# Kernel optimization log

Hardware: AMD Instinct MI355X
Metric: run time of the kernel (lower is better)

Reference implementation:

```python
import jax, jax.numpy as jnp
import numpy as np

N, E, FN, FE, L, G = 4096, 16384, 16, 8, 128, 64
EPS = 1e-5


def setup_inputs() -> dict:
    key = jax.random.key(0)
    ks = iter(jax.random.split(key, 40))

    def lin_w(shape):
        return jax.random.normal(next(ks), shape, jnp.float32) * (1.0 / np.sqrt(shape[0]))

    d = {}
    d["x"] = jax.random.normal(next(ks), (N, FN), jnp.float32)
    d["edge_attr"] = jax.random.normal(next(ks), (E, FE), jnp.float32)
    d["edge_index"] = jax.random.randint(next(ks), (2, E), 0, N)
    d["batch"] = jnp.sort(jax.random.randint(next(ks), (N,), 0, G))
    for i, (cin, cout) in enumerate([(FN, 32), (32, 64), (64, 128)], 1):
        d[f"We{i}"] = lin_w((FE, cin * cout))          # edge_fc weight
        d[f"be{i}"] = jnp.zeros((cin * cout,), jnp.float32)
        d[f"bias{i}"] = jnp.zeros((cout,), jnp.float32)
        d[f"Wr{i}"] = lin_w((cin, cout))               # res_fc weight
        d[f"br{i}"] = jnp.zeros((cout,), jnp.float32)
        d[f"bn_g{i}"] = jnp.ones((cout,), jnp.float32)
        d[f"bn_b{i}"] = jnp.zeros((cout,), jnp.float32)
        d[f"a{i}"] = jnp.float32(0.25)                  # PReLU slope
    d["Wi"] = lin_w((128, 128)); d["bi"] = jnp.zeros((128,), jnp.float32)
    d["Wj"] = lin_w((128, 128)); d["bj"] = jnp.zeros((128,), jnp.float32)
    d["Wfc"] = lin_w((128, 2 * L)); d["bfc"] = jnp.zeros((2 * L,), jnp.float32)
    return d


def _ecc(x, src, dst, norm, edge_attr, We, be, bias, Wr, br, cout, cin):
    # dynamically generated per-edge filter: [E, out, in]
    theta = (edge_attr @ We + be).reshape(E, cout, cin)
    # gather source features, per-edge matvec, degree-normalize (norm_j)
    msg = norm[src][:, None] * jnp.einsum('eoi,ei->eo', theta, x[src])
    # scatter-add into destination nodes + bias + residual linear
    return jax.ops.segment_sum(msg, dst, num_segments=N) + bias + x @ Wr + br


def _bn(x, g, b):
    m = x.mean(0)
    v = x.var(0)  # biased variance, as torch BN training normalization
    return (x - m) * jax.lax.rsqrt(v + EPS) * g + b


def _prelu(x, a):
    return jnp.where(x >= 0, x, a * x)


def reference(x, edge_attr, edge_index, batch,
              We1, be1, bias1, Wr1, br1, bn_g1, bn_b1, a1,
              We2, be2, bias2, Wr2, br2, bn_g2, bn_b2, a2,
              We3, be3, bias3, Wr3, br3, bn_g3, bn_b3, a3,
              Wi, bi, Wj, bj, Wfc, bfc):
    src, dst = edge_index[0], edge_index[1]
    deg = jax.ops.segment_sum(jnp.ones((E,), x.dtype), src, num_segments=N)
    norm = jnp.where(deg > 0, 1.0 / deg, 0.0)

    h = _ecc(x, src, dst, norm, edge_attr, We1, be1, bias1, Wr1, br1, 32, FN)
    h = _prelu(_bn(h, bn_g1, bn_b1), a1)
    h = _ecc(h, src, dst, norm, edge_attr, We2, be2, bias2, Wr2, br2, 64, 32)
    h = _prelu(_bn(h, bn_g2, bn_b2), a2)
    h = _ecc(h, src, dst, norm, edge_attr, We3, be3, bias3, Wr3, br3, 128, 64)
    h = _prelu(_bn(h, bn_g3, bn_b3), a3)

    # gated attention pooling (GGS-NN eq. 7), scatter-sum per graph
    gates = jax.nn.sigmoid(h @ Wi + bi)
    feats = jnp.tanh(h @ Wj + bj)
    pooled = jnp.tanh(jax.ops.segment_sum(gates * feats, batch, num_segments=G))

    z = pooled @ Wfc + bfc  # [G, 2L]
    return z[:, :L], z[:, L:]
```

## Files before the change

kernel.cpp:

```cpp
#include <hip/hip_runtime.h>
#include <math.h>

#define NN 4096
#define NE 16384
#define NG 64

#define OFF_DEG   0
#define OFF_ST1   4096
#define OFF_ST2   4160
#define OFF_ST3   4288
#define OFF_POOL  4544
#define ZERO_FLOATS 12736
#define OFF_H1    12736
#define OFF_H2    143808
#define OFF_H3    405952
#define OFF_Y     930240

template<int K, int COUT, bool BN, bool DEG>
__global__ __launch_bounds__(256) void k_proj(
    const float* __restrict__ A,
    const float* __restrict__ We, const float* __restrict__ be,
    const float* __restrict__ Wr, const float* __restrict__ bias,
    const float* __restrict__ br,
    const int* __restrict__ ei, float* __restrict__ deg,
    float* __restrict__ Y, float* __restrict__ h,
    const float* __restrict__ st, const float* __restrict__ g,
    const float* __restrict__ b, const float* __restrict__ a)
{
    constexpr int NCOL = 10 * COUT;
    constexpr int NY = NCOL / 64;
    constexpr int NC9 = 9 * COUT;
    constexpr int L2C = (COUT == 32) ? 5 : (COUT == 64) ? 6 : 7;

    const int tid = threadIdx.x;
    const int bid = blockIdx.x;

    if constexpr (DEG) {
        if (bid >= 64 * NY) {
            int e = (bid - 64 * NY) * 256 + tid;
            if (e < NE) atomicAdd(&deg[ei[e]], 1.0f);
            return;
        }
    }

    __shared__ float sA[K][68];
    __shared__ float sB[K][68];
    __shared__ float sS[K];
    __shared__ float sT[K];
    const int m0 = (bid & 63) * 64;
    const int n0 = (bid >> 6) * 64;

    float al = 0.f;
    if constexpr (BN) {
        if (tid < K) {
            float mean = st[tid] * (1.f / NN);
            float var  = st[K + tid] * (1.f / NN) - mean * mean;
            var = fmaxf(var, 0.f);
            float s = rsqrtf(var + 1e-5f) * g[tid];
            sS[tid] = s;
            sT[tid] = b[tid] - mean * s;
        }
        al = a[0];
        __syncthreads();
    }

    for (int t = tid; t < 64 * K; t += 256) {
        int m = t / K, i = t - m * K;
        float v = A[(m0 + m) * K + i];
        if constexpr (BN) {
            v = fmaf(v, sS[i], sT[i]);
            v = v >= 0.f ? v : al * v;
        }
        sA[i][m] = v;
    }
    for (int t = tid; t < 64 * K; t += 256) {
        int i = t >> 6, n = t & 63;
        int col = n0 + n;
        int f = col >> L2C;
        int o = col & (COUT - 1);
        float v;
        if (f < 8)       v = We[f * K * COUT + o * K + i];
        else if (f == 8) v = be[o * K + i];
        else             v = Wr[i * COUT + o];
        sB[i][n] = v;
    }
    __syncthreads();

    const int tn = tid & 15, tm = tid >> 4;
    float acc[4][4] = {{0.f}};
#pragma unroll 8
    for (int i = 0; i < K; ++i) {
        float4 av = *(const float4*)&sA[i][tm * 4];
        float4 bv = *(const float4*)&sB[i][tn * 4];
        acc[0][0] += av.x * bv.x; acc[0][1] += av.x * bv.y; acc[0][2] += av.x * bv.z; acc[0][3] += av.x * bv.w;
        acc[1][0] += av.y * bv.x; acc[1][1] += av.y * bv.y; acc[1][2] += av.y * bv.z; acc[1][3] += av.y * bv.w;
        acc[2][0] += av.z * bv.x; acc[2][1] += av.z * bv.y; acc[2][2] += av.z * bv.z; acc[2][3] += av.z * bv.w;
        acc[3][0] += av.w * bv.x; acc[3][1] += av.w * bv.y; acc[3][2] += av.w * bv.z; acc[3][3] += av.w * bv.w;
    }

#pragma unroll
    for (int mm = 0; mm < 4; ++mm) {
        int m = m0 + tm * 4 + mm;
#pragma unroll
        for (int nn = 0; nn < 4; ++nn) {
            int col = n0 + tn * 4 + nn;
            if (col < NC9) {
                Y[(size_t)m * NC9 + col] = acc[mm][nn];
            } else {
                int o = col - NC9;
                h[m * COUT + o] = acc[mm][nn] + bias[o] + br[o];
            }
        }
    }
}

template<int COUT>
__global__ __launch_bounds__(256) void k_egather(
    const float* __restrict__ Y, const float* __restrict__ eattr,
    const int* __restrict__ ei, const float* __restrict__ deg,
    float* __restrict__ h)
{
    int idx = blockIdx.x * 256 + threadIdx.x;
    int e = idx / COUT;
    int o = idx - e * COUT;
    int src = ei[e], dst = ei[NE + e];
    float d = deg[src];
    float nrm = d > 0.f ? 1.f / d : 0.f;
    const float* y = Y + (size_t)src * (9 * COUT);
    const float* ea = eattr + e * 8;
    float acc = y[8 * COUT + o];
#pragma unroll
    for (int f = 0; f < 8; ++f) acc += ea[f] * y[f * COUT + o];
    atomicAdd(&h[dst * COUT + o], nrm * acc);
}

template<int COUT>
__global__ __launch_bounds__(256) void k_stats(
    const float* __restrict__ h, float* __restrict__ st)
{
    constexpr int NL = 256 / COUT;
    constexpr int KN = 16 / NL;
    __shared__ float sred[256];
    const int tid = threadIdx.x;
    const int nbase = blockIdx.x * 16;
    const int o = tid % COUT;
    const int nl = tid / COUT;

    float sum = 0.f, sumsq = 0.f;
#pragma unroll
    for (int k = 0; k < KN; ++k) {
        int r = nl * KN + k;
        float v = h[(nbase + r) * COUT + o];
        sum += v; sumsq += v * v;
    }
    sred[tid] = sum;
    __syncthreads();
    if (tid < COUT) {
        float s = 0.f;
        for (int q = 0; q < NL; ++q) s += sred[q * COUT + tid];
        atomicAdd(&st[tid], s);
    }
    __syncthreads();
    sred[tid] = sumsq;
    __syncthreads();
    if (tid < COUT) {
        float s = 0.f;
        for (int q = 0; q < NL; ++q) s += sred[q * COUT + tid];
        atomicAdd(&st[COUT + tid], s);
    }
}

__global__ __launch_bounds__(256) void k_pool(
    const float* __restrict__ h3, const int* __restrict__ batch,
    const float* __restrict__ Wi, const float* __restrict__ bi,
    const float* __restrict__ Wj, const float* __restrict__ bj,
    float* __restrict__ pooled,
    const float* __restrict__ st, const float* __restrict__ g,
    const float* __restrict__ b, const float* __restrict__ a)
{
    constexpr int KN = 8, NB = 16;
    __shared__ float sH[NB * 128];
    __shared__ int sB[NB];
    __shared__ float sS[128];
    __shared__ float sT[128];
    const int tid = threadIdx.x;
    const int nbase = blockIdx.x * NB;

    if (tid < 128) {
        float mean = st[tid] * (1.f / NN);
        float var  = st[128 + tid] * (1.f / NN) - mean * mean;
        var = fmaxf(var, 0.f);
        float s = rsqrtf(var + 1e-5f) * g[tid];
        sS[tid] = s;
        sT[tid] = b[tid] - mean * s;
    }
    if (tid < NB) sB[tid] = batch[nbase + tid];
    __syncthreads();
    const float al = a[0];

    for (int t = tid; t < NB * 128; t += 256) {
        int c = t & 127;
        float v = h3[nbase * 128 + t];
        v = fmaf(v, sS[c], sT[c]);
        v = v >= 0.f ? v : al * v;
        sH[t] = v;
    }
    __syncthreads();

    const int o = tid & 127, nl = tid >> 7;
    float gacc[KN], facc[KN];
#pragma unroll
    for (int k = 0; k < KN; ++k) { gacc[k] = 0.f; facc[k] = 0.f; }
    for (int i = 0; i < 128; ++i) {
        float wi = Wi[i * 128 + o], wj = Wj[i * 128 + o];
#pragma unroll
        for (int k = 0; k < KN; ++k) {
            float hv = sH[(nl * KN + k) * 128 + i];
            gacc[k] += hv * wi;
            facc[k] += hv * wj;
        }
    }
    float bio = bi[o], bjo = bj[o];
    float psum = 0.f;
    int curg = sB[nl * KN];
#pragma unroll
    for (int k = 0; k < KN; ++k) {
        int r = nl * KN + k;
        int bg = sB[r];
        if (bg != curg) {
            atomicAdd(&pooled[curg * 128 + o], psum);
            psum = 0.f; curg = bg;
        }
        float gate = 1.f / (1.f + expf(-(gacc[k] + bio)));
        float feat = tanhf(facc[k] + bjo);
        psum += gate * feat;
    }
    atomicAdd(&pooled[curg * 128 + o], psum);
}

__global__ __launch_bounds__(256) void k_final(
    const float* __restrict__ pooled, const float* __restrict__ Wfc,
    const float* __restrict__ bfc, float* __restrict__ out)
{
    __shared__ float sP[128];
    const int g = blockIdx.x, c = threadIdx.x;
    if (c < 128) sP[c] = tanhf(pooled[g * 128 + c]);
    __syncthreads();
    float z = bfc[c];
    for (int i = 0; i < 128; ++i) z += sP[i] * Wfc[i * 256 + c];
    int oidx = (c < 128) ? (g * 128 + c) : (NG * 128 + g * 128 + (c - 128));
    out[oidx] = z;
}

extern "C" void kernel_launch(void* const* d_in, const int* in_sizes, int n_in,
                              void* d_out, int out_size, void* d_ws, size_t ws_size,
                              hipStream_t stream)
{
    (void)in_sizes; (void)n_in; (void)out_size; (void)ws_size;
    const float* x     = (const float*)d_in[0];
    const float* eattr = (const float*)d_in[1];
    const int*   ei    = (const int*)d_in[2];
    const int*   batch = (const int*)d_in[3];
    const float* We1 = (const float*)d_in[4];
    const float* be1 = (const float*)d_in[5];
    const float* bias1 = (const float*)d_in[6];
    const float* Wr1 = (const float*)d_in[7];
    const float* br1 = (const float*)d_in[8];
    const float* bg1 = (const float*)d_in[9];
    const float* bb1 = (const float*)d_in[10];
    const float* a1  = (const float*)d_in[11];
    const float* We2 = (const float*)d_in[12];
    const float* be2 = (const float*)d_in[13];
    const float* bias2 = (const float*)d_in[14];
    const float* Wr2 = (const float*)d_in[15];
    const float* br2 = (const float*)d_in[16];
    const float* bg2 = (const float*)d_in[17];
    const float* bb2 = (const float*)d_in[18];
    const float* a2  = (const float*)d_in[19];
    const float* We3 = (const float*)d_in[20];
    const float* be3 = (const float*)d_in[21];
    const float* bias3 = (const float*)d_in[22];
    const float* Wr3 = (const float*)d_in[23];
    const float* br3 = (const float*)d_in[24];
    const float* bg3 = (const float*)d_in[25];
    const float* bb3 = (const float*)d_in[26];
    const float* a3  = (const float*)d_in[27];
    const float* Wi  = (const float*)d_in[28];
    const float* bi  = (const float*)d_in[29];
    const float* Wj  = (const float*)d_in[30];
    const float* bj  = (const float*)d_in[31];
    const float* Wfc = (const float*)d_in[32];
    const float* bfc = (const float*)d_in[33];
    float* ws  = (float*)d_ws;
    float* out = (float*)d_out;

    hipMemsetAsync(d_ws, 0, (size_t)ZERO_FLOATS * sizeof(float), stream);

    k_proj<16, 32, false, true><<<64 * 5 + 64, 256, 0, stream>>>(
        x, We1, be1, Wr1, bias1, br1, ei, ws + OFF_DEG,
        ws + OFF_Y, ws + OFF_H1, nullptr, nullptr, nullptr, nullptr);
    k_egather<32><<<NE * 32 / 256, 256, 0, stream>>>(
        ws + OFF_Y, eattr, ei, ws + OFF_DEG, ws + OFF_H1);
    k_stats<32><<<NN / 16, 256, 0, stream>>>(ws + OFF_H1, ws + OFF_ST1);

    k_proj<32, 64, true, false><<<64 * 10, 256, 0, stream>>>(
        ws + OFF_H1, We2, be2, Wr2, bias2, br2, nullptr, nullptr,
        ws + OFF_Y, ws + OFF_H2, ws + OFF_ST1, bg1, bb1, a1);
    k_egather<64><<<NE * 64 / 256, 256, 0, stream>>>(
        ws + OFF_Y, eattr, ei, ws + OFF_DEG, ws + OFF_H2);
    k_stats<64><<<NN / 16, 256, 0, stream>>>(ws + OFF_H2, ws + OFF_ST2);

    k_proj<64, 128, true, false><<<64 * 20, 256, 0, stream>>>(
        ws + OFF_H2, We3, be3, Wr3, bias3, br3, nullptr, nullptr,
        ws + OFF_Y, ws + OFF_H3, ws + OFF_ST2, bg2, bb2, a2);
    k_egather<128><<<NE * 128 / 256, 256, 0, stream>>>(
        ws + OFF_Y, eattr, ei, ws + OFF_DEG, ws + OFF_H3);
    k_stats<128><<<NN / 16, 256, 0, stream>>>(ws + OFF_H3, ws + OFF_ST3);

    k_pool<<<NN / 16, 256, 0, stream>>>(ws + OFF_H3, batch, Wi, bi, Wj, bj, ws + OFF_POOL,
                                        ws + OFF_ST3, bg3, bb3, a3);
    k_final<<<NG, 256, 0, stream>>>(ws + OFF_POOL, Wfc, bfc, out);
}
```

Before: 240.5 us.

## Fuse gather+stats and pool+final kernels via atomic counter gates

Merges each edge-gather kernel with the following BN-stats kernel, and the pooling kernel with the final linear kernel, into single launches. Later blocks spin on a global atomic counter until all producer blocks have posted completion. This removes four kernel launches and their launch gaps. It relies on producer blocks being scheduled before or alongside the waiting consumer blocks, which risks deadlock if consumers occupy all slots, and adds spin-wait cost.

```diff
diff --git a/kernel.cpp b/kernel.cpp
--- a/kernel.cpp
+++ b/kernel.cpp
@@ -10,11 +10,27 @@
 #define OFF_ST2   4160
 #define OFF_ST3   4288
 #define OFF_POOL  4544
-#define ZERO_FLOATS 12736
-#define OFF_H1    12736
-#define OFF_H2    143808
-#define OFF_H3    405952
-#define OFF_Y     930240
+#define OFF_CNT   12736
+#define ZERO_FLOATS 12752
+#define OFF_H1    12752
+#define OFF_H2    143824
+#define OFF_H3    405968
+#define OFF_Y     930256
+
+__device__ __forceinline__ void gate_post(int* cnt) {
+    asm volatile("s_waitcnt vmcnt(0)" ::: "memory");
+    __syncthreads();
+    if (threadIdx.x == 0)
+        __hip_atomic_fetch_add(cnt, 1, __ATOMIC_RELEASE, __HIP_MEMORY_SCOPE_AGENT);
+}
+__device__ __forceinline__ void gate_wait(int* cnt, int target) {
+    if (threadIdx.x == 0) {
+        while (__hip_atomic_load(cnt, __ATOMIC_RELAXED, __HIP_MEMORY_SCOPE_AGENT) < target)
+            __builtin_amdgcn_s_sleep(8);
+        (void)__hip_atomic_load(cnt, __ATOMIC_ACQUIRE, __HIP_MEMORY_SCOPE_AGENT);
+    }
+    __syncthreads();
+}
 
 template<int K, int COUT, bool BN, bool DEG>
 __global__ __launch_bounds__(256) void k_proj(
@@ -114,35 +130,37 @@
     }
 }
 
-template<int COUT>
-__global__ __launch_bounds__(256) void k_egather(
+template<int COUT, int NEGB>
+__global__ __launch_bounds__(256) void k_egstats(
     const float* __restrict__ Y, const float* __restrict__ eattr,
     const int* __restrict__ ei, const float* __restrict__ deg,
-    float* __restrict__ h)
+    float* __restrict__ h, float* __restrict__ st, int* __restrict__ cnt)
 {
-    int idx = blockIdx.x * 256 + threadIdx.x;
-    int e = idx / COUT;
-    int o = idx - e * COUT;
-    int src = ei[e], dst = ei[NE + e];
-    float d = deg[src];
-    float nrm = d > 0.f ? 1.f / d : 0.f;
-    const float* y = Y + (size_t)src * (9 * COUT);
-    const float* ea = eattr + e * 8;
-    float acc = y[8 * COUT + o];
-#pragma unroll
-    for (int f = 0; f < 8; ++f) acc += ea[f] * y[f * COUT + o];
-    atomicAdd(&h[dst * COUT + o], nrm * acc);
-}
-
-template<int COUT>
-__global__ __launch_bounds__(256) void k_stats(
-    const float* __restrict__ h, float* __restrict__ st)
-{
+    const int tid = threadIdx.x;
+    const int bid = blockIdx.x;
+    __shared__ float sred[256];
+
+    if (bid < NEGB) {
+        int idx = bid * 256 + tid;
+        int e = idx / COUT;
+        int o = idx - e * COUT;
+        int src = ei[e], dst = ei[NE + e];
+        float d = deg[src];
+        float nrm = d > 0.f ? 1.f / d : 0.f;
+        const float* y = Y + (size_t)src * (9 * COUT);
+        const float* ea = eattr + e * 8;
+        float acc = y[8 * COUT + o];
+#pragma unroll
+        for (int f = 0; f < 8; ++f) acc += ea[f] * y[f * COUT + o];
+        atomicAdd(&h[dst * COUT + o], nrm * acc);
+        gate_post(cnt);
+        return;
+    }
+
+    gate_wait(cnt, NEGB);
     constexpr int NL = 256 / COUT;
     constexpr int KN = 16 / NL;
-    __shared__ float sred[256];
-    const int tid = threadIdx.x;
-    const int nbase = blockIdx.x * 16;
+    const int nbase = (bid - NEGB) * 16;
     const int o = tid % COUT;
     const int nl = tid / COUT;
 
@@ -170,13 +188,15 @@
     }
 }
 
-__global__ __launch_bounds__(256) void k_pool(
+__global__ __launch_bounds__(256) void k_poolfinal(
     const float* __restrict__ h3, const int* __restrict__ batch,
     const float* __restrict__ Wi, const float* __restrict__ bi,
     const float* __restrict__ Wj, const float* __restrict__ bj,
     float* __restrict__ pooled,
     const float* __restrict__ st, const float* __restrict__ g,
-    const float* __restrict__ b, const float* __restrict__ a)
+    const float* __restrict__ b, const float* __restrict__ a,
+    const float* __restrict__ Wfc, const float* __restrict__ bfc,
+    float* __restrict__ out, int* __restrict__ cnt)
 {
     constexpr int KN = 8, NB = 16;
     __shared__ float sH[NB * 128];
@@ -184,71 +204,72 @@
     __shared__ float sS[128];
     __shared__ float sT[128];
     const int tid = threadIdx.x;
-    const int nbase = blockIdx.x * NB;
-
-    if (tid < 128) {
-        float mean = st[tid] * (1.f / NN);
-        float var  = st[128 + tid] * (1.f / NN) - mean * mean;
-        var = fmaxf(var, 0.f);
-        float s = rsqrtf(var + 1e-5f) * g[tid];
-        sS[tid] = s;
-        sT[tid] = b[tid] - mean * s;
-    }
-    if (tid < NB) sB[tid] = batch[nbase + tid];
-    __syncthreads();
-    const float al = a[0];
-
-    for (int t = tid; t < NB * 128; t += 256) {
-        int c = t & 127;
-        float v = h3[nbase * 128 + t];
-        v = fmaf(v, sS[c], sT[c]);
-        v = v >= 0.f ? v : al * v;
-        sH[t] = v;
-    }
-    __syncthreads();
-
-    const int o = tid & 127, nl = tid >> 7;
-    float gacc[KN], facc[KN];
-#pragma unroll
-    for (int k = 0; k < KN; ++k) { gacc[k] = 0.f; facc[k] = 0.f; }
-    for (int i = 0; i < 128; ++i) {
-        float wi = Wi[i * 128 + o], wj = Wj[i * 128 + o];
+    const int bid = blockIdx.x;
+
+    if (bid < 256) {
+        const int nbase = bid * NB;
+        if (tid < 128) {
+            float mean = st[tid] * (1.f / NN);
+            float var  = st[128 + tid] * (1.f / NN) - mean * mean;
+            var = fmaxf(var, 0.f);
+            float s = rsqrtf(var + 1e-5f) * g[tid];
+            sS[tid] = s;
+            sT[tid] = b[tid] - mean * s;
+        }
+        if (tid < NB) sB[tid] = batch[nbase + tid];
+        __syncthreads();
+        const float al = a[0];
+
+        for (int t = tid; t < NB * 128; t += 256) {
+            int c = t & 127;
+            float v = h3[nbase * 128 + t];
+            v = fmaf(v, sS[c], sT[c]);
+            v = v >= 0.f ? v : al * v;
+            sH[t] = v;
+        }
+        __syncthreads();
+
+        const int o = tid & 127, nl = tid >> 7;
+        float gacc[KN], facc[KN];
+#pragma unroll
+        for (int k = 0; k < KN; ++k) { gacc[k] = 0.f; facc[k] = 0.f; }
+        for (int i = 0; i < 128; ++i) {
+            float wi = Wi[i * 128 + o], wj = Wj[i * 128 + o];
+#pragma unroll
+            for (int k = 0; k < KN; ++k) {
+                float hv = sH[(nl * KN + k) * 128 + i];
+                gacc[k] += hv * wi;
+                facc[k] += hv * wj;
+            }
+        }
+        float bio = bi[o], bjo = bj[o];
+        float psum = 0.f;
+        int curg = sB[nl * KN];
 #pragma unroll
         for (int k = 0; k < KN; ++k) {
-            float hv = sH[(nl * KN + k) * 128 + i];
-            gacc[k] += hv * wi;
-            facc[k] += hv * wj;
-        }
-    }
-    float bio = bi[o], bjo = bj[o];
-    float psum = 0.f;
-    int curg = sB[nl * KN];
-#pragma unroll
-    for (int k = 0; k < KN; ++k) {
-        int r = nl * KN + k;
-        int bg = sB[r];
-        if (bg != curg) {
-            atomicAdd(&pooled[curg * 128 + o], psum);
-            psum = 0.f; curg = bg;
-        }
-        float gate = 1.f / (1.f + expf(-(gacc[k] + bio)));
-        float feat = tanhf(facc[k] + bjo);
-        psum += gate * feat;
-    }
-    atomicAdd(&pooled[curg * 128 + o], psum);
-}
-
-__global__ __launch_bounds__(256) void k_final(
-    const float* __restrict__ pooled, const float* __restrict__ Wfc,
-    const float* __restrict__ bfc, float* __restrict__ out)
-{
-    __shared__ float sP[128];
-    const int g = blockIdx.x, c = threadIdx.x;
-    if (c < 128) sP[c] = tanhf(pooled[g * 128 + c]);
-    __syncthreads();
-    float z = bfc[c];
-    for (int i = 0; i < 128; ++i) z += sP[i] * Wfc[i * 256 + c];
-    int oidx = (c < 128) ? (g * 128 + c) : (NG * 128 + g * 128 + (c - 128));
+            int r = nl * KN + k;
+            int bg = sB[r];
+            if (bg != curg) {
+                atomicAdd(&pooled[curg * 128 + o], psum);
+                psum = 0.f; curg = bg;
+            }
+            float gate = 1.f / (1.f + expf(-(gacc[k] + bio)));
+            float feat = tanhf(facc[k] + bjo);
+            psum += gate * feat;
+        }
+        atomicAdd(&pooled[curg * 128 + o], psum);
+        gate_post(cnt);
+        return;
+    }
+
+    gate_wait(cnt, 256);
+    float* sP = sS;
+    const int gid = bid - 256;
+    if (tid < 128) sP[tid] = tanhf(pooled[gid * 128 + tid]);
+    __syncthreads();
+    float z = bfc[tid];
+    for (int i = 0; i < 128; ++i) z += sP[i] * Wfc[i * 256 + tid];
+    int oidx = (tid < 128) ? (gid * 128 + tid) : (NG * 128 + gid * 128 + (tid - 128));
     out[oidx] = z;
 }
 
@@ -293,31 +314,29 @@
     const float* bfc = (const float*)d_in[33];
     float* ws  = (float*)d_ws;
     float* out = (float*)d_out;
+    int* cnt = (int*)(ws + OFF_CNT);
 
     hipMemsetAsync(d_ws, 0, (size_t)ZERO_FLOATS * sizeof(float), stream);
 
     k_proj<16, 32, false, true><<<64 * 5 + 64, 256, 0, stream>>>(
         x, We1, be1, Wr1, bias1, br1, ei, ws + OFF_DEG,
         ws + OFF_Y, ws + OFF_H1, nullptr, nullptr, nullptr, nullptr);
-    k_egather<32><<<NE * 32 / 256, 256, 0, stream>>>(
-        ws + OFF_Y, eattr, ei, ws + OFF_DEG, ws + OFF_H1);
-    k_stats<32><<<NN / 16, 256, 0, stream>>>(ws + OFF_H1, ws + OFF_ST1);
+    k_egstats<32, NE * 32 / 256><<<NE * 32 / 256 + 256, 256, 0, stream>>>(
+        ws + OFF_Y, eattr, ei, ws + OFF_DEG, ws + OFF_H1, ws + OFF_ST1, cnt + 0);
 
     k_proj<32, 64, true, false><<<64 * 10, 256, 0, stream>>>(
         ws + OFF_H1, We2, be2, Wr2, bias2, br2, nullptr, nullptr,
         ws + OFF_Y, ws + OFF_H2, ws + OFF_ST1, bg1, bb1, a1);
-    k_egather<64><<<NE * 64 / 256, 256, 0, stream>>>(
-        ws + OFF_Y, eattr, ei, ws + OFF_DEG, ws + OFF_H2);
-    k_stats<64><<<NN / 16, 256, 0, stream>>>(ws + OFF_H2, ws + OFF_ST2);
+    k_egstats<64, NE * 64 / 256><<<NE * 64 / 256 + 256, 256, 0, stream>>>(
+        ws + OFF_Y, eattr, ei, ws + OFF_DEG, ws + OFF_H2, ws + OFF_ST2, cnt + 1);
 
     k_proj<64, 128, true, false><<<64 * 20, 256, 0, stream>>>(
         ws + OFF_H2, We3, be3, Wr3, bias3, br3, nullptr, nullptr,
         ws + OFF_Y, ws + OFF_H3, ws + OFF_ST2, bg2, bb2, a2);
-    k_egather<128><<<NE * 128 / 256, 256, 0, stream>>>(
-        ws + OFF_Y, eattr, ei, ws + OFF_DEG, ws + OFF_H3);
-    k_stats<128><<<NN / 16, 256, 0, stream>>>(ws + OFF_H3, ws + OFF_ST3);
-
-    k_pool<<<NN / 16, 256, 0, stream>>>(ws + OFF_H3, batch, Wi, bi, Wj, bj, ws + OFF_POOL,
-                                        ws + OFF_ST3, bg3, bb3, a3);
-    k_final<<<NG, 256, 0, stream>>>(ws + OFF_POOL, Wfc, bfc, out);
-}
+    k_egstats<128, NE * 128 / 256><<<NE * 128 / 256 + 256, 256, 0, stream>>>(
+        ws + OFF_Y, eattr, ei, ws + OFF_DEG, ws + OFF_H3, ws + OFF_ST3, cnt + 2);
+
+    k_poolfinal<<<256 + NG, 256, 0, stream>>>(
+        ws + OFF_H3, batch, Wi, bi, Wj, bj, ws + OFF_POOL,
+        ws + OFF_ST3, bg3, bb3, a3, Wfc, bfc, out, cnt + 3);
+}
```

Result: slower. 709.2 us (+194.9%).
